# Kernel tuning notes

Hardware: AMD Instinct MI355X
Metric: run time of the kernel (lower is better)

Reference implementation:

```python
import jax, jax.numpy as jnp
import numpy as np

NUM_NODES = 100000
NUM_EDGES = 1600000
FEAT = 128
HID = 128
NUM_GRAPHS = 512


def setup_inputs() -> dict:
    key = jax.random.key(0)
    ks = jax.random.split(key, 8)
    x = jax.random.normal(ks[0], (NUM_NODES, FEAT), dtype=jnp.float32)
    edge_index = jax.random.randint(ks[1], (2, NUM_EDGES), 0, NUM_NODES, dtype=jnp.int64)
    batch = jnp.sort(jax.random.randint(ks[2], (NUM_NODES,), 0, NUM_GRAPHS, dtype=jnp.int64))
    # Glorot-ish init for weights (scale named for clarity)
    s1 = 1.0 / np.sqrt(FEAT)
    s2 = 1.0 / np.sqrt(HID)
    W1 = jax.random.normal(ks[3], (FEAT, HID), dtype=jnp.float32) * s1
    b1 = jnp.zeros((HID,), dtype=jnp.float32)
    W2 = jax.random.normal(ks[4], (HID, HID), dtype=jnp.float32) * s2
    b2 = jnp.zeros((HID,), dtype=jnp.float32)
    Wout = jax.random.normal(ks[5], (HID, 1), dtype=jnp.float32) * s2
    bout = jnp.zeros((1,), dtype=jnp.float32)
    return {"x": x, "edge_index": edge_index, "batch": batch,
            "W1": W1, "b1": b1, "W2": W2, "b2": b2, "Wout": Wout, "bout": bout}


def reference(x, edge_index, batch, W1, b1, W2, b2, Wout, bout):
    N = x.shape[0]
    # PyG GCNConv: add self-loops, symmetric normalization D^-1/2 (A+I) D^-1/2
    loops = jnp.arange(N, dtype=edge_index.dtype)
    src = jnp.concatenate([edge_index[0], loops])  # [E+N]
    dst = jnp.concatenate([edge_index[1], loops])  # [E+N]
    ones = jnp.ones_like(dst, dtype=x.dtype)
    deg = jax.ops.segment_sum(ones, dst, num_segments=N)  # in-degree incl. self-loop
    dinv = jnp.where(deg > 0, jax.lax.rsqrt(deg), 0.0)
    coeff = (dinv[src] * dinv[dst])[:, None]  # [E+N, 1]

    def gcn(h, W, b):
        h = h @ W                                       # [N, H] dense GEMM
        msg = h[src] * coeff                            # gather + scale
        agg = jax.ops.segment_sum(msg, dst, num_segments=N)  # scatter-add
        return agg + b

    h = jax.nn.relu(gcn(x, W1, b1))
    h = jax.nn.relu(gcn(h, W2, b2))

    # global_mean_pool over batch ids
    G = NUM_GRAPHS
    sums = jax.ops.segment_sum(h, batch, num_segments=G)
    cnts = jax.ops.segment_sum(jnp.ones((N,), dtype=h.dtype), batch, num_segments=G)
    pooled = sums / jnp.maximum(cnts, 1.0)[:, None]

    return pooled @ Wout + bout  # [G, 1]
```

## Files before the change

kernel.cpp:

```cpp
#include <hip/hip_runtime.h>
#include <hip/hip_bf16.h>
#include <hip/hip_fp16.h>

#define FEAT 128
#define PSLOTS 64
#define BCAP 5120

typedef _Float16 h8 __attribute__((ext_vector_type(8)));
typedef float f4 __attribute__((ext_vector_type(4)));


__global__ __launch_bounds__(256) void k_bin(const int* __restrict__ ei, int E, int chunk,
                                             int* __restrict__ cursor,
                                             unsigned* __restrict__ binned, int nb,
                                             const float* __restrict__ W1,
                                             const float* __restrict__ W2,
                                             __half* __restrict__ Wt1,
                                             __half* __restrict__ Wt2) {
    if (blockIdx.x >= 256) {
        int t = (blockIdx.x - 256) * 256 + threadIdx.x;
        const float* W = (t < 8192) ? W1 : W2;
        __half* Wt     = (t < 8192) ? Wt1 : Wt2;
        int u = t & 8191;
        int n = u >> 6, k2 = (u & 63) * 2;
        float a = W[(size_t)k2 * 128 + n];
        float b = W[(size_t)(k2 + 1) * 128 + n];
        ((__half2*)Wt)[n * 64 + (k2 >> 1)] = __floats2half2_rn(a, b);
        return;
    }
    __shared__ int hist[512];
    __shared__ int base[512];
    int start = blockIdx.x * chunk;
    int end = start + chunk; if (end > E) end = E;
    for (int i = threadIdx.x; i < nb; i += 256) hist[i] = 0;
    __syncthreads();
    for (int e = start + threadIdx.x; e < end; e += 256)
        atomicAdd(&hist[ei[E + e] >> 8], 1);
    __syncthreads();
    for (int i = threadIdx.x; i < nb; i += 256) {
        int h = hist[i];
        base[i] = h ? atomicAdd(&cursor[i], h) : 0;
    }
    __syncthreads();
    for (int e = start + threadIdx.x; e < end; e += 256) {
        int s = ei[e];
        int d = ei[E + e];
        int b = d >> 8;
        int pos = atomicAdd(&base[b], 1);
        if (pos < BCAP)
            binned[(size_t)b * BCAP + pos] = (unsigned)s | ((unsigned)(d & 255) << 17);
    }
}


__global__ __launch_bounds__(256) void k_deg_fill(const unsigned* __restrict__ binned,
                                                  const int* __restrict__ cursor,
                                                  int N, int* __restrict__ deg,
                                                  int* __restrict__ rowstart,
                                                  float* __restrict__ dinv,
                                                  int* __restrict__ meta) {
    __shared__ int ld[256];
    __shared__ int sc[256];
    __shared__ int cur[256];
    int b = blockIdx.x;
    int cnt = cursor[b]; if (cnt > BCAP) cnt = BCAP;
    int s = b * BCAP, e = s + cnt;
    ld[threadIdx.x] = 0;
    __syncthreads();
    for (int i = s + threadIdx.x; i < e; i += 256)
        atomicAdd(&ld[binned[i] >> 17], 1);
    __syncthreads();
    int d = ld[threadIdx.x];
    sc[threadIdx.x] = d;
    __syncthreads();
    for (int off = 1; off < 256; off <<= 1) {
        int t = (threadIdx.x >= off) ? sc[threadIdx.x - off] : 0;
        __syncthreads();
        sc[threadIdx.x] += t;
        __syncthreads();
    }
    int rs = s + sc[threadIdx.x] - d;
    cur[threadIdx.x] = rs;
    int v = (b << 8) + threadIdx.x;
    if (v < N) {
        deg[v] = d;
        rowstart[v] = rs;
        dinv[v] = rsqrtf((float)d + 1.0f);
    }
    __syncthreads();
    for (int i = s + threadIdx.x; i < e; i += 256) {
        unsigned p = binned[i];
        int src = (int)(p & 0x1FFFF);
        int drl = (int)(p >> 17);
        int pos = atomicAdd(&cur[drl], 1);
        meta[pos] = src << 8;
    }
}


__device__ __forceinline__ void loadA(const __half* p, int quad, h8* a) {
#pragma unroll
    for (int ks = 0; ks < 4; ++ks)
        a[ks] = *(const h8*)(p + ks * 32 + quad * 8);
}
__device__ __forceinline__ void loadA(const float* p, int quad, h8* a) {
#pragma unroll
    for (int ks = 0; ks < 4; ++ks) {
        const float* q = p + ks * 32 + quad * 8;
        float4 f0 = *(const float4*)q;
        float4 f1 = *(const float4*)(q + 4);
        h8 v;
        v[0] = (_Float16)f0.x; v[1] = (_Float16)f0.y;
        v[2] = (_Float16)f0.z; v[3] = (_Float16)f0.w;
        v[4] = (_Float16)f1.x; v[5] = (_Float16)f1.y;
        v[6] = (_Float16)f1.z; v[7] = (_Float16)f1.w;
        a[ks] = v;
    }
}

template <typename TIN>
__global__ __launch_bounds__(256) void gemm_mfma(const TIN* __restrict__ X,
                                                 const __half* __restrict__ Wt,
                                                 __half* __restrict__ Y, int N) {
    __shared__ _Float16 Bs[128 * 128];
    {
        const float4* src = (const float4*)Wt;
        float4* dst = (float4*)Bs;
        for (int i = threadIdx.x; i < 2048; i += 256) {
            int n = i >> 4, ch = i & 15;
            dst[n * 16 + (ch ^ (n & 15))] = src[i];
        }
    }
    __syncthreads();

    int lane = threadIdx.x & 63;
    int wave = threadIdx.x >> 6;
    int m = lane & 15;
    int quad = lane >> 4;
    int rowb = blockIdx.x * 128 + wave * 16;

    h8 a[2][4];
#pragma unroll
    for (int rt = 0; rt < 2; ++rt) {
        int rA = rowb + rt * 64 + m; if (rA >= N) rA = N - 1;
        loadA(X + (size_t)rA * FEAT, quad, a[rt]);
    }

    f4 acc[2][8];
#pragma unroll
    for (int rt = 0; rt < 2; ++rt)
#pragma unroll
        for (int nt = 0; nt < 8; ++nt) acc[rt][nt] = (f4){0.f, 0.f, 0.f, 0.f};

#pragma unroll
    for (int nt = 0; nt < 8; ++nt) {
        const _Float16* bbase = Bs + (nt * 16 + m) * 128;
#pragma unroll
        for (int ks = 0; ks < 4; ++ks) {
            int ch = (ks * 4 + quad) ^ m;
            h8 bfrag = *(const h8*)(bbase + ch * 8);
            acc[0][nt] = __builtin_amdgcn_mfma_f32_16x16x32_f16(a[0][ks], bfrag, acc[0][nt], 0, 0, 0);
            acc[1][nt] = __builtin_amdgcn_mfma_f32_16x16x32_f16(a[1][ks], bfrag, acc[1][nt], 0, 0, 0);
        }
    }

#pragma unroll
    for (int rt = 0; rt < 2; ++rt)
#pragma unroll
    for (int nt = 0; nt < 8; ++nt) {
#pragma unroll
        for (int r = 0; r < 4; ++r) {
            int row = rowb + rt * 64 + quad * 4 + r;
            if (row < N)
                Y[(size_t)row * FEAT + nt * 16 + m] = __float2half(acc[rt][nt][r]);
        }
    }
}


template <bool POOL>
__global__ __launch_bounds__(256) void agg_relu(const __half* __restrict__ Y,
                                                const float* __restrict__ dinv,
                                                const int* __restrict__ rowstart,
                                                const int* __restrict__ degc,
                                                const int* __restrict__ meta,
                                                const float* __restrict__ bias,
                                                __half* __restrict__ H, int N,
                                                const float* __restrict__ Wout,
                                                const int* __restrict__ batch,
                                                float* __restrict__ gsum, int G) {
    int wid  = (blockIdx.x * 256 + threadIdx.x) >> 6;
    int lane = threadIdx.x & 63;
    if (wid >= N) return;
    int v = wid;
    float dv = dinv[v];

    const char* Yb = (const char*)Y;
    int lb = lane * 4;

    float2 yv = __half22float2(((const __half2*)(Y + (size_t)v * FEAT))[lane]);
    float selfc = dv * dv;
    float accx = selfc * yv.x;
    float accy = selfc * yv.y;

    int base = rowstart[v];
    int n = degc[v];
    for (int i0 = 0; i0 < n; i0 += 64) {
        int m = n - i0; if (m > 64) m = 64;
        int sl = 0; float cl = 0.f;
        if (lane < m) {
            sl = meta[base + i0 + lane];
            cl = dinv[sl >> 8] * dv;
        }
        for (int i = 0; i < m; i += 8) {
            int   o0 = __shfl(sl, i + 0), o1 = __shfl(sl, i + 1);
            int   o2 = __shfl(sl, i + 2), o3 = __shfl(sl, i + 3);
            int   o4 = __shfl(sl, i + 4), o5 = __shfl(sl, i + 5);
            int   o6 = __shfl(sl, i + 6), o7 = __shfl(sl, i + 7);
            float c0 = __shfl(cl, i + 0), c1 = __shfl(cl, i + 1);
            float c2 = __shfl(cl, i + 2), c3 = __shfl(cl, i + 3);
            float c4 = __shfl(cl, i + 4), c5 = __shfl(cl, i + 5);
            float c6 = __shfl(cl, i + 6), c7 = __shfl(cl, i + 7);
            float2 y0 = __half22float2(*(const __half2*)(Yb + o0 + lb));
            float2 y1 = __half22float2(*(const __half2*)(Yb + o1 + lb));
            float2 y2 = __half22float2(*(const __half2*)(Yb + o2 + lb));
            float2 y3 = __half22float2(*(const __half2*)(Yb + o3 + lb));
            float2 y4 = __half22float2(*(const __half2*)(Yb + o4 + lb));
            float2 y5 = __half22float2(*(const __half2*)(Yb + o5 + lb));
            float2 y6 = __half22float2(*(const __half2*)(Yb + o6 + lb));
            float2 y7 = __half22float2(*(const __half2*)(Yb + o7 + lb));
            accx += c0 * y0.x; accy += c0 * y0.y;
            accx += c1 * y1.x; accy += c1 * y1.y;
            accx += c2 * y2.x; accy += c2 * y2.y;
            accx += c3 * y3.x; accy += c3 * y3.y;
            accx += c4 * y4.x; accy += c4 * y4.y;
            accx += c5 * y5.x; accy += c5 * y5.y;
            accx += c6 * y6.x; accy += c6 * y6.y;
            accx += c7 * y7.x; accy += c7 * y7.y;
        }
    }
    float2 b = ((const float2*)bias)[lane];
    float hx = fmaxf(accx + b.x, 0.f);
    float hy = fmaxf(accy + b.y, 0.f);
    if (POOL) {
        float2 wo = ((const float2*)Wout)[lane];
        float s = hx * wo.x + hy * wo.y;
        s += __shfl_xor(s, 1);
        s += __shfl_xor(s, 2);
        s += __shfl_xor(s, 4);
        s += __shfl_xor(s, 8);
        s += __shfl_xor(s, 16);
        s += __shfl_xor(s, 32);
        if (lane == 0) {
            int slot = blockIdx.x & (PSLOTS - 1);
            atomicAdd(&gsum[slot * G + batch[v]], s);
        }
    } else {
        ((__half2*)(H + (size_t)v * FEAT))[lane] = __floats2half2_rn(hx, hy);
    }
}


__global__ __launch_bounds__(256) void k_head(const float* __restrict__ gsum,
                                              const int* __restrict__ batch, int N, int G,
                                              const float* __restrict__ bout,
                                              float* __restrict__ out) {
    int g = blockIdx.x * 256 + threadIdx.x;
    if (g >= G) return;
    float s = 0.f;
#pragma unroll 8
    for (int k = 0; k < PSLOTS; ++k) s += gsum[k * G + g];
    int lo = 0, hi = N;
    while (lo < hi) { int mid = (lo + hi) >> 1; if (batch[mid] < g) lo = mid + 1; else hi = mid; }
    int start = lo;
    lo = start; hi = N;
    while (lo < hi) { int mid = (lo + hi) >> 1; if (batch[mid] < g + 1) lo = mid + 1; else hi = mid; }
    int cnt = lo - start;
    out[g] = s / (float)(cnt > 0 ? cnt : 1) + bout[0];
}


extern "C" void kernel_launch(void* const* d_in, const int* in_sizes, int n_in,
                              void* d_out, int out_size, void* d_ws, size_t ws_size,
                              hipStream_t stream) {
    const float* x    = (const float*)d_in[0];
    const int*   ei   = (const int*)d_in[1];
    const int*   batch= (const int*)d_in[2];
    const float* W1   = (const float*)d_in[3];
    const float* b1   = (const float*)d_in[4];
    const float* W2   = (const float*)d_in[5];
    const float* b2   = (const float*)d_in[6];
    const float* Wout = (const float*)d_in[7];
    const float* bout = (const float*)d_in[8];

    int N = in_sizes[0] / FEAT;
    int E = in_sizes[1] / 2;
    int G = out_size;
    int nb = (N + 255) >> 8;

    char* ws = (char*)d_ws;
    size_t off = 0;
    auto alloc = [&](size_t bytes) -> void* {
        void* p = ws + off;
        off += (bytes + 255) & ~(size_t)255;
        return p;
    };
    __half* bufA     = (__half*)alloc((size_t)N * FEAT * 2);
    __half* bufB     = (__half*)alloc((size_t)N * FEAT * 2);
    __half* Wt1      = (__half*)alloc((size_t)FEAT * FEAT * 2);
    __half* Wt2      = (__half*)alloc((size_t)FEAT * FEAT * 2);
    float* dinv      = (float*)alloc((size_t)N * 4);
    int*   deg       = (int*)alloc((size_t)N * 4);
    int*   rowstart  = (int*)alloc((size_t)N * 4);
    float* gsum      = (float*)alloc((size_t)PSLOTS * G * 4 + (size_t)nb * 4);
    int*   cursor    = (int*)(gsum + (size_t)PSLOTS * G);
    unsigned* binned = (unsigned*)alloc((size_t)nb * BCAP * 4);
    int*   meta      = (int*)alloc((size_t)nb * BCAP * 4);

    hipMemsetAsync(gsum, 0, (size_t)PSLOTS * G * 4 + (size_t)nb * 4, stream);
    int chunk = (E + 255) / 256;
    k_bin<<<320, 256, 0, stream>>>(ei, E, chunk, cursor, binned, nb, W1, W2, Wt1, Wt2);
    k_deg_fill<<<nb, 256, 0, stream>>>(binned, cursor, N, deg, rowstart, dinv, meta);

    int gemm_grid = (N + 127) / 128;
    int agg_grid  = (N + 3) / 4;

    gemm_mfma<float><<<gemm_grid, 256, 0, stream>>>(x, Wt1, bufA, N);
    agg_relu<false><<<agg_grid, 256, 0, stream>>>(bufA, dinv, rowstart, deg, meta, b1, bufB, N,
                                                  nullptr, nullptr, nullptr, 0);
    gemm_mfma<__half><<<gemm_grid, 256, 0, stream>>>(bufB, Wt2, bufA, N);
    agg_relu<true><<<agg_grid, 256, 0, stream>>>(bufA, dinv, rowstart, deg, meta, b2, nullptr, N,
                                                 Wout, batch, gsum, G);
    k_head<<<(G + 255) / 256, 256, 0, stream>>>(gsum, batch, N, G, bout, (float*)d_out);
}
```

Before: 314.1 us.

## Co-schedule first-layer GEMM with edge binning in one launch

Splits the weight transpose into its own small kernel, then merges the first-layer MFMA GEMM and the edge-binning pass into a single kernel whose blocks branch by block index. The GEMM (compute and x-streaming) and the binning (atomics and scattered writes) are independent, so running them concurrently is meant to overlap their latencies and remove one launch gap. In exchange, shared memory per block becomes 32KB for the binning blocks too, and the extra small weight-transpose kernel must finish before the fused launch.

```diff
diff --git a/kernel.cpp b/kernel.cpp
--- a/kernel.cpp
+++ b/kernel.cpp
@@ -10,27 +10,28 @@
 typedef float f4 __attribute__((ext_vector_type(4)));
 
 
-__global__ __launch_bounds__(256) void k_bin(const int* __restrict__ ei, int E, int chunk,
-                                             int* __restrict__ cursor,
-                                             unsigned* __restrict__ binned, int nb,
-                                             const float* __restrict__ W1,
-                                             const float* __restrict__ W2,
-                                             __half* __restrict__ Wt1,
-                                             __half* __restrict__ Wt2) {
-    if (blockIdx.x >= 256) {
-        int t = (blockIdx.x - 256) * 256 + threadIdx.x;
-        const float* W = (t < 8192) ? W1 : W2;
-        __half* Wt     = (t < 8192) ? Wt1 : Wt2;
-        int u = t & 8191;
-        int n = u >> 6, k2 = (u & 63) * 2;
-        float a = W[(size_t)k2 * 128 + n];
-        float b = W[(size_t)(k2 + 1) * 128 + n];
-        ((__half2*)Wt)[n * 64 + (k2 >> 1)] = __floats2half2_rn(a, b);
-        return;
-    }
-    __shared__ int hist[512];
-    __shared__ int base[512];
-    int start = blockIdx.x * chunk;
+__global__ __launch_bounds__(256) void k_wt(const float* __restrict__ W1,
+                                            const float* __restrict__ W2,
+                                            __half* __restrict__ Wt1,
+                                            __half* __restrict__ Wt2) {
+    int t = blockIdx.x * 256 + threadIdx.x;
+    const float* W = (t < 8192) ? W1 : W2;
+    __half* Wt     = (t < 8192) ? Wt1 : Wt2;
+    int u = t & 8191;
+    int n = u >> 6, k2 = (u & 63) * 2;
+    float a = W[(size_t)k2 * 128 + n];
+    float b = W[(size_t)(k2 + 1) * 128 + n];
+    ((__half2*)Wt)[n * 64 + (k2 >> 1)] = __floats2half2_rn(a, b);
+}
+
+
+__device__ __forceinline__ void bin_body(const int* __restrict__ ei, int E, int chunk,
+                                         int* __restrict__ cursor,
+                                         unsigned* __restrict__ binned, int nb,
+                                         int bid, int* smem) {
+    int* hist = smem;
+    int* base = smem + 512;
+    int start = bid * chunk;
     int end = start + chunk; if (end > E) end = E;
     for (int i = threadIdx.x; i < nb; i += 256) hist[i] = 0;
     __syncthreads();
@@ -50,6 +51,109 @@
         if (pos < BCAP)
             binned[(size_t)b * BCAP + pos] = (unsigned)s | ((unsigned)(d & 255) << 17);
     }
+}
+
+
+__device__ __forceinline__ void loadA(const __half* p, int quad, h8* a) {
+#pragma unroll
+    for (int ks = 0; ks < 4; ++ks)
+        a[ks] = *(const h8*)(p + ks * 32 + quad * 8);
+}
+__device__ __forceinline__ void loadA(const float* p, int quad, h8* a) {
+#pragma unroll
+    for (int ks = 0; ks < 4; ++ks) {
+        const float* q = p + ks * 32 + quad * 8;
+        float4 f0 = *(const float4*)q;
+        float4 f1 = *(const float4*)(q + 4);
+        h8 v;
+        v[0] = (_Float16)f0.x; v[1] = (_Float16)f0.y;
+        v[2] = (_Float16)f0.z; v[3] = (_Float16)f0.w;
+        v[4] = (_Float16)f1.x; v[5] = (_Float16)f1.y;
+        v[6] = (_Float16)f1.z; v[7] = (_Float16)f1.w;
+        a[ks] = v;
+    }
+}
+
+template <typename TIN>
+__device__ __forceinline__ void gemm_body(const TIN* __restrict__ X,
+                                          const __half* __restrict__ Wt,
+                                          __half* __restrict__ Y, int N,
+                                          int bid, _Float16* Bs) {
+    {
+        const float4* src = (const float4*)Wt;
+        float4* dst = (float4*)Bs;
+        for (int i = threadIdx.x; i < 2048; i += 256) {
+            int n = i >> 4, ch = i & 15;
+            dst[n * 16 + (ch ^ (n & 15))] = src[i];
+        }
+    }
+    __syncthreads();
+
+    int lane = threadIdx.x & 63;
+    int wave = threadIdx.x >> 6;
+    int m = lane & 15;
+    int quad = lane >> 4;
+    int rowb = bid * 128 + wave * 16;
+
+    h8 a[2][4];
+#pragma unroll
+    for (int rt = 0; rt < 2; ++rt) {
+        int rA = rowb + rt * 64 + m; if (rA >= N) rA = N - 1;
+        loadA(X + (size_t)rA * FEAT, quad, a[rt]);
+    }
+
+    f4 acc[2][8];
+#pragma unroll
+    for (int rt = 0; rt < 2; ++rt)
+#pragma unroll
+        for (int nt = 0; nt < 8; ++nt) acc[rt][nt] = (f4){0.f, 0.f, 0.f, 0.f};
+
+#pragma unroll
+    for (int nt = 0; nt < 8; ++nt) {
+        const _Float16* bbase = Bs + (nt * 16 + m) * 128;
+#pragma unroll
+        for (int ks = 0; ks < 4; ++ks) {
+            int ch = (ks * 4 + quad) ^ m;
+            h8 bfrag = *(const h8*)(bbase + ch * 8);
+            acc[0][nt] = __builtin_amdgcn_mfma_f32_16x16x32_f16(a[0][ks], bfrag, acc[0][nt], 0, 0, 0);
+            acc[1][nt] = __builtin_amdgcn_mfma_f32_16x16x32_f16(a[1][ks], bfrag, acc[1][nt], 0, 0, 0);
+        }
+    }
+
+#pragma unroll
+    for (int rt = 0; rt < 2; ++rt)
+#pragma unroll
+    for (int nt = 0; nt < 8; ++nt) {
+#pragma unroll
+        for (int r = 0; r < 4; ++r) {
+            int row = rowb + rt * 64 + quad * 4 + r;
+            if (row < N)
+                Y[(size_t)row * FEAT + nt * 16 + m] = __float2half(acc[rt][nt][r]);
+        }
+    }
+}
+
+
+__global__ __launch_bounds__(256) void gemm_bin(const float* __restrict__ X,
+                                                const __half* __restrict__ Wt1,
+                                                __half* __restrict__ Y, int N, int gemm_grid,
+                                                const int* __restrict__ ei, int E, int chunk,
+                                                int* __restrict__ cursor,
+                                                unsigned* __restrict__ binned, int nb) {
+    __shared__ __align__(16) char smem[32768];
+    if ((int)blockIdx.x < gemm_grid)
+        gemm_body<float>(X, Wt1, Y, N, blockIdx.x, (_Float16*)smem);
+    else
+        bin_body(ei, E, chunk, cursor, binned, nb, blockIdx.x - gemm_grid, (int*)smem);
+}
+
+
+template <typename TIN>
+__global__ __launch_bounds__(256) void gemm_mfma(const TIN* __restrict__ X,
+                                                 const __half* __restrict__ Wt,
+                                                 __half* __restrict__ Y, int N) {
+    __shared__ __align__(16) _Float16 Bs[128 * 128];
+    gemm_body<TIN>(X, Wt, Y, N, blockIdx.x, Bs);
 }
 
 
@@ -94,86 +198,6 @@
         int drl = (int)(p >> 17);
         int pos = atomicAdd(&cur[drl], 1);
         meta[pos] = src << 8;
-    }
-}
-
-
-__device__ __forceinline__ void loadA(const __half* p, int quad, h8* a) {
-#pragma unroll
-    for (int ks = 0; ks < 4; ++ks)
-        a[ks] = *(const h8*)(p + ks * 32 + quad * 8);
-}
-__device__ __forceinline__ void loadA(const float* p, int quad, h8* a) {
-#pragma unroll
-    for (int ks = 0; ks < 4; ++ks) {
-        const float* q = p + ks * 32 + quad * 8;
-        float4 f0 = *(const float4*)q;
-        float4 f1 = *(const float4*)(q + 4);
-        h8 v;
-        v[0] = (_Float16)f0.x; v[1] = (_Float16)f0.y;
-        v[2] = (_Float16)f0.z; v[3] = (_Float16)f0.w;
-        v[4] = (_Float16)f1.x; v[5] = (_Float16)f1.y;
-        v[6] = (_Float16)f1.z; v[7] = (_Float16)f1.w;
-        a[ks] = v;
-    }
-}
-
-template <typename TIN>
-__global__ __launch_bounds__(256) void gemm_mfma(const TIN* __restrict__ X,
-                                                 const __half* __restrict__ Wt,
-                                                 __half* __restrict__ Y, int N) {
-    __shared__ _Float16 Bs[128 * 128];
-    {
-        const float4* src = (const float4*)Wt;
-        float4* dst = (float4*)Bs;
-        for (int i = threadIdx.x; i < 2048; i += 256) {
-            int n = i >> 4, ch = i & 15;
-            dst[n * 16 + (ch ^ (n & 15))] = src[i];
-        }
-    }
-    __syncthreads();
-
-    int lane = threadIdx.x & 63;
-    int wave = threadIdx.x >> 6;
-    int m = lane & 15;
-    int quad = lane >> 4;
-    int rowb = blockIdx.x * 128 + wave * 16;
-
-    h8 a[2][4];
-#pragma unroll
-    for (int rt = 0; rt < 2; ++rt) {
-        int rA = rowb + rt * 64 + m; if (rA >= N) rA = N - 1;
-        loadA(X + (size_t)rA * FEAT, quad, a[rt]);
-    }
-
-    f4 acc[2][8];
-#pragma unroll
-    for (int rt = 0; rt < 2; ++rt)
-#pragma unroll
-        for (int nt = 0; nt < 8; ++nt) acc[rt][nt] = (f4){0.f, 0.f, 0.f, 0.f};
-
-#pragma unroll
-    for (int nt = 0; nt < 8; ++nt) {
-        const _Float16* bbase = Bs + (nt * 16 + m) * 128;
-#pragma unroll
-        for (int ks = 0; ks < 4; ++ks) {
-            int ch = (ks * 4 + quad) ^ m;
-            h8 bfrag = *(const h8*)(bbase + ch * 8);
-            acc[0][nt] = __builtin_amdgcn_mfma_f32_16x16x32_f16(a[0][ks], bfrag, acc[0][nt], 0, 0, 0);
-            acc[1][nt] = __builtin_amdgcn_mfma_f32_16x16x32_f16(a[1][ks], bfrag, acc[1][nt], 0, 0, 0);
-        }
-    }
-
-#pragma unroll
-    for (int rt = 0; rt < 2; ++rt)
-#pragma unroll
-    for (int nt = 0; nt < 8; ++nt) {
-#pragma unroll
-        for (int r = 0; r < 4; ++r) {
-            int row = rowb + rt * 64 + quad * 4 + r;
-            if (row < N)
-                Y[(size_t)row * FEAT + nt * 16 + m] = __float2half(acc[rt][nt][r]);
-        }
     }
 }
 
@@ -317,15 +341,15 @@
     unsigned* binned = (unsigned*)alloc((size_t)nb * BCAP * 4);
     int*   meta      = (int*)alloc((size_t)nb * BCAP * 4);
 
-    hipMemsetAsync(gsum, 0, (size_t)PSLOTS * G * 4 + (size_t)nb * 4, stream);
-    int chunk = (E + 255) / 256;
-    k_bin<<<320, 256, 0, stream>>>(ei, E, chunk, cursor, binned, nb, W1, W2, Wt1, Wt2);
-    k_deg_fill<<<nb, 256, 0, stream>>>(binned, cursor, N, deg, rowstart, dinv, meta);
-
     int gemm_grid = (N + 127) / 128;
     int agg_grid  = (N + 3) / 4;
-
-    gemm_mfma<float><<<gemm_grid, 256, 0, stream>>>(x, Wt1, bufA, N);
+    int chunk = (E + 255) / 256;
+
+    hipMemsetAsync(gsum, 0, (size_t)PSLOTS * G * 4 + (size_t)nb * 4, stream);
+    k_wt<<<64, 256, 0, stream>>>(W1, W2, Wt1, Wt2);
+    gemm_bin<<<gemm_grid + 256, 256, 0, stream>>>(x, Wt1, bufA, N, gemm_grid,
+                                                  ei, E, chunk, cursor, binned, nb);
+    k_deg_fill<<<nb, 256, 0, stream>>>(binned, cursor, N, deg, rowstart, dinv, meta);
     agg_relu<false><<<agg_grid, 256, 0, stream>>>(bufA, dinv, rowstart, deg, meta, b1, bufB, N,
                                                   nullptr, nullptr, nullptr, 0);
     gemm_mfma<__half><<<gemm_grid, 256, 0, stream>>>(bufB, Wt2, bufA, N);
```

Result: faster. 307.7 us (-2.0%).
